# Optimization experiments

Hardware: AMD Instinct MI355X
Metric: run time of the kernel (lower is better)

Reference implementation:

```python
import jax, jax.numpy as jnp
import numpy as np

N_NODES = 100000
N_EDGES = 1600000
IN_DIM = 128
HEADS = 4
HEAD_DIM = 16  # hidden_dim 64 // 4 heads
HID = HEADS * HEAD_DIM
NEG_SLOPE = 0.2


def setup_inputs() -> dict:
    key = jax.random.key(0)
    ks = jax.random.split(key, 20)
    inp = {
        "x": jax.random.normal(ks[0], (N_NODES, IN_DIM), dtype=jnp.float32),
        "edge_index": jax.random.randint(ks[1], (2, N_EDGES), 0, N_NODES, dtype=jnp.int32),
    }
    dims = [IN_DIM, HID, HID]
    for l in range(3):
        d_in = dims[l]
        sc = 1.0 / np.sqrt(d_in)
        inp[f"w{l}"] = jax.random.normal(ks[2 + 4 * l], (d_in, HID), dtype=jnp.float32) * sc
        inp[f"asrc{l}"] = jax.random.normal(ks[3 + 4 * l], (HEADS, HEAD_DIM), dtype=jnp.float32) * 0.1
        inp[f"adst{l}"] = jax.random.normal(ks[4 + 4 * l], (HEADS, HEAD_DIM), dtype=jnp.float32) * 0.1
        inp[f"b{l}"] = jnp.zeros((HID,), dtype=jnp.float32)
    inp["out_w"] = jax.random.normal(ks[14], (HID, 1), dtype=jnp.float32) * (1.0 / np.sqrt(HID))
    inp["out_b"] = jnp.zeros((1,), dtype=jnp.float32)
    return inp


def _gat_layer(h, src, dst, W, a_src, a_dst, b):
    # h: [N, d_in]; src/dst: [E'] (self-loops already appended)
    n = h.shape[0]
    xh = (h @ W).reshape(n, HEADS, HEAD_DIM)              # [N,H,C]
    al_s = jnp.sum(xh * a_src, axis=-1)                   # [N,H]
    al_d = jnp.sum(xh * a_dst, axis=-1)                   # [N,H]
    e = jax.nn.leaky_relu(al_s[src] + al_d[dst], NEG_SLOPE)  # [E',H]
    # segment-softmax over incoming edges of each destination node
    m = jax.ops.segment_max(e, dst, num_segments=n)       # [N,H]
    p = jnp.exp(e - m[dst])
    z = jax.ops.segment_sum(p, dst, num_segments=n)       # [N,H]
    alpha = p / (z[dst] + 1e-16)                          # [E',H]
    msg = xh[src] * alpha[:, :, None]                     # [E',H,C]
    out = jax.ops.segment_sum(msg, dst, num_segments=n)   # [N,H,C]
    return out.reshape(n, HID) + b


def reference(x, edge_index, w0, asrc0, adst0, b0, w1, asrc1, adst1, b1,
              w2, asrc2, adst2, b2, out_w, out_b):
    n = x.shape[0]
    loops = jnp.arange(n, dtype=edge_index.dtype)
    src = jnp.concatenate([edge_index[0], loops])  # PyG GATConv adds self-loops
    dst = jnp.concatenate([edge_index[1], loops])
    h = x
    params = [(w0, asrc0, adst0, b0), (w1, asrc1, adst1, b1), (w2, asrc2, adst2, b2)]
    for W, a_s, a_d, b in params:
        h = _gat_layer(h, src, dst, W, a_s, a_d, b)
        h = jax.nn.relu(h)
    return (h @ out_w + out_b).squeeze(-1)  # [N]
```

## Files before the change

kernel.cpp:

```cpp
#include <hip/hip_runtime.h>


#define NBMAX 512
#define SCHUNK 4096
#define BCAP 8192

typedef __attribute__((ext_vector_type(8))) short bf16x8;
typedef __attribute__((ext_vector_type(4))) float f32x4;

__device__ inline unsigned short bf16_rtn(float x) {
    union { float f; unsigned u; } a; a.f = x;
    return (unsigned short)((a.u + 0x7FFFu + ((a.u >> 16) & 1u)) >> 16);
}
__device__ inline float bf16_to_f(unsigned short s) {
    union { unsigned u; float f; } b; b.u = ((unsigned)s) << 16;
    return b.f;
}

__global__ __launch_bounds__(256) void k_zero(int* p, int n) {
    int i = blockIdx.x * 256 + threadIdx.x;
    if (i < n) p[i] = 0;
}

__global__ __launch_bounds__(256) void k_bhist(const int* __restrict__ dst, int* __restrict__ bhist, int e) {
    __shared__ unsigned int h[NBMAX];
    int t = threadIdx.x;
    h[t] = 0;
    h[t + 256] = 0;
    __syncthreads();
    for (int i = blockIdx.x * 256 + t; i < e; i += gridDim.x * 256)
        atomicAdd(&h[dst[i] >> 8], 1u);
    __syncthreads();
    if (h[t]) atomicAdd(&bhist[t], (int)h[t]);
    if (h[t + 256]) atomicAdd(&bhist[t + 256], (int)h[t + 256]);
}

__global__ __launch_bounds__(512) void k_bscan(const int* __restrict__ bhist, int* __restrict__ boffs,
                                               int* __restrict__ bfill, int nb, int e) {
    __shared__ int s[NBMAX];
    int t = threadIdx.x;
    int v = (t < nb) ? bhist[t] : 0;
    s[t] = v;
    __syncthreads();
    for (int o = 1; o < 512; o <<= 1) {
        int add = (t >= o) ? s[t - o] : 0;
        __syncthreads();
        s[t] += add;
        __syncthreads();
    }
    boffs[t] = s[t] - v;
    if (t == 511) boffs[512] = s[511];
    bfill[t] = 0;
}

__global__ __launch_bounds__(512) void k_bscatter(const int* __restrict__ src, const int* __restrict__ dst,
                                                  const int* __restrict__ boffs, int* __restrict__ bfill,
                                                  unsigned int* __restrict__ edata, int e) {
    __shared__ unsigned int hist[NBMAX];
    __shared__ unsigned int loc[NBMAX];
    __shared__ int gbase[NBMAX];
    __shared__ unsigned int stmp[NBMAX];
    __shared__ unsigned int sortbuf[SCHUNK];
    __shared__ int posbuf[SCHUNK];
    int t = threadIdx.x;
    int i0 = blockIdx.x * SCHUNK;
    int cnt = min(SCHUNK, e - i0);
    hist[t] = 0;
    __syncthreads();
    for (int j = t; j < cnt; j += 512) atomicAdd(&hist[dst[i0 + j] >> 8], 1u);
    __syncthreads();
    unsigned int v = hist[t];
    stmp[t] = v;
    __syncthreads();
    for (int o = 1; o < 512; o <<= 1) {
        unsigned int add = (t >= o) ? stmp[t - o] : 0;
        __syncthreads();
        stmp[t] += add;
        __syncthreads();
    }
    loc[t] = stmp[t] - v;
    int gb = 0;
    if (v > 0) gb = atomicAdd(&bfill[t], (int)v);
    gbase[t] = boffs[t] + gb - (int)loc[t];
    hist[t] = loc[t];
    __syncthreads();
    for (int j = t; j < cnt; j += 512) {
        int d = dst[i0 + j];
        int s = src[i0 + j];
        int b = d >> 8;
        unsigned int p = atomicAdd(&hist[b], 1u);
        sortbuf[p] = (unsigned int)s | ((unsigned int)(d & 255) << 24);
        posbuf[p] = gbase[b] + (int)p;
    }
    __syncthreads();
    for (int j = t; j < cnt; j += 512) edata[posbuf[j]] = sortbuf[j];
}

__global__ __launch_bounds__(256) void k_bfinal(const unsigned int* __restrict__ edata,
                                                const int* __restrict__ boffs, int* __restrict__ offs,
                                                int* __restrict__ ssrc, int* __restrict__ sdst,
                                                int n, int nb) {
    __shared__ unsigned int hist[256];
    __shared__ unsigned int stmp[256];
    __shared__ unsigned int loc[256];
    __shared__ unsigned int srcbuf[BCAP];
    __shared__ unsigned char dstbuf[BCAP];
    int b = blockIdx.x;
    int t = threadIdx.x;
    int e0 = boffs[b], e1 = boffs[b + 1];
    int cnt = e1 - e0;
    hist[t] = 0;
    __syncthreads();
    for (int j = t; j < cnt; j += 256) atomicAdd(&hist[edata[e0 + j] >> 24], 1u);
    __syncthreads();
    unsigned int v = hist[t];
    stmp[t] = v;
    __syncthreads();
    for (int o = 1; o < 256; o <<= 1) {
        unsigned int add = (t >= o) ? stmp[t - o] : 0;
        __syncthreads();
        stmp[t] += add;
        __syncthreads();
    }
    loc[t] = stmp[t] - v;
    int node = b * 256 + t;
    if (node < n) offs[node] = e0 + (int)loc[t];
    if (b == nb - 1 && t == 0) offs[n] = e1;
    hist[t] = loc[t];
    __syncthreads();
    if (cnt <= BCAP) {
        for (int j = t; j < cnt; j += 256) {
            unsigned int p = edata[e0 + j];
            unsigned int pos = atomicAdd(&hist[p >> 24], 1u);
            srcbuf[pos] = p & 0xFFFFFFu;
            dstbuf[pos] = (unsigned char)(p >> 24);
        }
        __syncthreads();
        for (int j = t; j < cnt; j += 256) {
            ssrc[e0 + j] = (int)srcbuf[j];
            sdst[e0 + j] = b * 256 + (int)dstbuf[j];
        }
    } else {
        for (int j = t; j < cnt; j += 256) {
            unsigned int p = edata[e0 + j];
            unsigned int pos = atomicAdd(&hist[p >> 24], 1u);
            ssrc[e0 + (int)pos] = (int)(p & 0xFFFFFFu);
            sdst[e0 + (int)pos] = b * 256 + (int)(p >> 24);
        }
    }
}

__global__ __launch_bounds__(256) void k_wprep(const float* __restrict__ w0, const float* __restrict__ w1,
                                               const float* __restrict__ w2,
                                               unsigned short* __restrict__ p0h, unsigned short* __restrict__ p0l,
                                               unsigned short* __restrict__ p1h, unsigned short* __restrict__ p1l,
                                               unsigned short* __restrict__ p2h, unsigned short* __restrict__ p2l) {
    int g = blockIdx.x * 256 + threadIdx.x;
    const float* W;
    unsigned short *ph, *pl;
    int idx;
    if (g < 1024) { W = w0; ph = p0h; pl = p0l; idx = g; }
    else if (g < 1536) { W = w1; ph = p1h; pl = p1l; idx = g - 1024; }
    else if (g < 2048) { W = w2; ph = p2h; pl = p2l; idx = g - 1536; }
    else return;
    int ko = idx >> 6, nn = idx & 63;
#pragma unroll
    for (int j = 0; j < 8; ++j) {
        float w = W[(size_t)(ko * 8 + j) * 64 + nn];
        unsigned short hb = bf16_rtn(w);
        ph[(size_t)idx * 8 + j] = hb;
        pl[(size_t)idx * 8 + j] = bf16_rtn(w - bf16_to_f(hb));
    }
}

template <int D_IN>
__global__ __launch_bounds__(256) void k_mgemm(const float* __restrict__ h,
                                               const unsigned short* __restrict__ wph,
                                               const unsigned short* __restrict__ wpl,
                                               const float* __restrict__ asrc, const float* __restrict__ adst,
                                               float* __restrict__ xh, float* __restrict__ als,
                                               float* __restrict__ ald, int n) {
    int t = threadIdx.x;
    int wv = t >> 6, lane = t & 63;
    int quad = lane >> 4, l16 = lane & 15;
    int m0 = blockIdx.x * 64 + wv * 16;
    int node_a = m0 + l16;
    int mm = min(node_a, n - 1);
    const float* hrow = h + (size_t)mm * D_IN + quad * 8;

    f32x4 acc[4];
#pragma unroll
    for (int i = 0; i < 4; ++i) acc[i] = (f32x4){0.f, 0.f, 0.f, 0.f};

    constexpr int KSTEPS = D_IN / 32;
#pragma unroll
    for (int s = 0; s < KSTEPS; ++s) {
        float4 a0 = *(const float4*)(hrow + s * 32);
        float4 a1 = *(const float4*)(hrow + s * 32 + 4);
        float av[8] = {a0.x, a0.y, a0.z, a0.w, a1.x, a1.y, a1.z, a1.w};
        bf16x8 ahi, alo;
#pragma unroll
        for (int j = 0; j < 8; ++j) {
            unsigned short hb = bf16_rtn(av[j]);
            ahi[j] = (short)hb;
            alo[j] = (short)bf16_rtn(av[j] - bf16_to_f(hb));
        }
        const unsigned short* bbase = wph + ((size_t)((s * 4 + quad) * 64 + l16)) * 8;
        const unsigned short* bbasel = wpl + ((size_t)((s * 4 + quad) * 64 + l16)) * 8;
#pragma unroll
        for (int nt = 0; nt < 4; ++nt) {
            bf16x8 bhi = *(const bf16x8*)(bbase + (size_t)nt * 16 * 8);
            bf16x8 blo = *(const bf16x8*)(bbasel + (size_t)nt * 16 * 8);
            acc[nt] = __builtin_amdgcn_mfma_f32_16x16x32_bf16(ahi, bhi, acc[nt], 0, 0, 0);
            acc[nt] = __builtin_amdgcn_mfma_f32_16x16x32_bf16(ahi, blo, acc[nt], 0, 0, 0);
            acc[nt] = __builtin_amdgcn_mfma_f32_16x16x32_bf16(alo, bhi, acc[nt], 0, 0, 0);
        }
    }
#pragma unroll
    for (int nt = 0; nt < 4; ++nt) {
        float as_l = asrc[nt * 16 + l16];
        float ad_l = adst[nt * 16 + l16];
#pragma unroll
        for (int r = 0; r < 4; ++r) {
            int node = m0 + quad * 4 + r;
            float c = acc[nt][r];
            if (node < n) xh[(size_t)node * 64 + nt * 16 + l16] = c;
            float ps = c * as_l, pd = c * ad_l;
            ps += __shfl_xor(ps, 1, 64); pd += __shfl_xor(pd, 1, 64);
            ps += __shfl_xor(ps, 2, 64); pd += __shfl_xor(pd, 2, 64);
            ps += __shfl_xor(ps, 4, 64); pd += __shfl_xor(pd, 4, 64);
            ps += __shfl_xor(ps, 8, 64); pd += __shfl_xor(pd, 8, 64);
            if (l16 == 0 && node < n) {
                als[node * 4 + nt] = ps;
                ald[node * 4 + nt] = pd;
            }
        }
    }
}

__device__ inline float4 lrelu4(float4 v) {
    float4 r;
    r.x = v.x >= 0.f ? v.x : 0.2f * v.x;
    r.y = v.y >= 0.f ? v.y : 0.2f * v.y;
    r.z = v.z >= 0.f ? v.z : 0.2f * v.z;
    r.w = v.w >= 0.f ? v.w : 0.2f * v.w;
    return r;
}

__global__ __launch_bounds__(256) void k_edge(const int* __restrict__ ssrc, const int* __restrict__ sdst,
                                              const float* __restrict__ als, const float* __restrict__ ald,
                                              float* __restrict__ pei, int e) {
    int j = blockIdx.x * 256 + threadIdx.x;
    if (j >= e) return;
    int u = ssrc[j], d = sdst[j];
    float4 alu = *(const float4*)(als + 4 * (size_t)u);
    float4 asd = *(const float4*)(als + 4 * (size_t)d);
    float4 add4 = *(const float4*)(ald + 4 * (size_t)d);
    float4 m4 = lrelu4(make_float4(asd.x + add4.x, asd.y + add4.y, asd.z + add4.z, asd.w + add4.w));
    float4 e4 = lrelu4(make_float4(alu.x + add4.x, alu.y + add4.y, alu.z + add4.z, alu.w + add4.w));
    float4 pe;
    pe.x = __expf(e4.x - m4.x);
    pe.y = __expf(e4.y - m4.y);
    pe.z = __expf(e4.z - m4.z);
    pe.w = __expf(e4.w - m4.w);
    *(float4*)(pei + 4 * (size_t)j) = pe;
}

__global__ __launch_bounds__(256) void k_agg(const float* __restrict__ xh, const float* __restrict__ pei,
                                             const int* __restrict__ offs, const int* __restrict__ ssrc,
                                             const float* __restrict__ bias, float* __restrict__ hout,
                                             const float* __restrict__ outw, const float* __restrict__ outb,
                                             float* __restrict__ fout, int n) {
    __shared__ int s_u[4][64];
    __shared__ float s_pe[4][4][64];
    int wslot = threadIdx.x >> 6;
    int lane = threadIdx.x & 63;
    int v = (blockIdx.x * 256 + threadIdx.x) >> 6;
    if (v >= n) return;
    int head = lane >> 4;
    int* ub = s_u[wslot];
    float* per = s_pe[wslot][head];
    float* pew = &s_pe[wslot][0][lane];

    int start = offs[v], end = offs[v + 1];
    const char* xl = (const char*)(xh + lane);
    float acc = *(const float*)(xl + ((size_t)(unsigned)v << 8));
    float zsum = 0.f;

    for (int s0 = start; s0 < end; s0 += 64) {
        int cnt = min(64, end - s0);
        bool act = lane < cnt;
        int u = v;
        float4 pe = make_float4(0.f, 0.f, 0.f, 0.f);
        if (act) {
            u = ssrc[s0 + lane];
            pe = *(const float4*)(pei + 4 * (size_t)(s0 + lane));
        }
        ub[lane] = u << 8;
        pew[0] = pe.x;
        pew[64] = pe.y;
        pew[128] = pe.z;
        pew[192] = pe.w;
        int ng = (cnt + 3) >> 2;
        int g = 0;
        for (; g + 2 <= ng; g += 2) {
            int4 uu0 = *(const int4*)&ub[g * 4];
            int4 uu1 = *(const int4*)&ub[g * 4 + 4];
            float4 pp0 = *(const float4*)&per[g * 4];
            float4 pp1 = *(const float4*)&per[g * 4 + 4];
            float x0 = *(const float*)(xl + (size_t)(unsigned)uu0.x);
            float x1 = *(const float*)(xl + (size_t)(unsigned)uu0.y);
            float x2 = *(const float*)(xl + (size_t)(unsigned)uu0.z);
            float x3 = *(const float*)(xl + (size_t)(unsigned)uu0.w);
            float x4 = *(const float*)(xl + (size_t)(unsigned)uu1.x);
            float x5 = *(const float*)(xl + (size_t)(unsigned)uu1.y);
            float x6 = *(const float*)(xl + (size_t)(unsigned)uu1.z);
            float x7 = *(const float*)(xl + (size_t)(unsigned)uu1.w);
            zsum += pp0.x + pp0.y + pp0.z + pp0.w;
            zsum += pp1.x + pp1.y + pp1.z + pp1.w;
            acc += pp0.x * x0; acc += pp0.y * x1; acc += pp0.z * x2; acc += pp0.w * x3;
            acc += pp1.x * x4; acc += pp1.y * x5; acc += pp1.z * x6; acc += pp1.w * x7;
        }
        for (; g < ng; ++g) {
            int4 uu = *(const int4*)&ub[g * 4];
            float4 pp = *(const float4*)&per[g * 4];
            float x0 = *(const float*)(xl + (size_t)(unsigned)uu.x);
            float x1 = *(const float*)(xl + (size_t)(unsigned)uu.y);
            float x2 = *(const float*)(xl + (size_t)(unsigned)uu.z);
            float x3 = *(const float*)(xl + (size_t)(unsigned)uu.w);
            zsum += pp.x + pp.y + pp.z + pp.w;
            acc += pp.x * x0; acc += pp.y * x1; acc += pp.z * x2; acc += pp.w * x3;
        }
    }
    float z = 1.f + zsum;
    float o = acc / (z + 1e-16f) + bias[lane];
    o = fmaxf(o, 0.f);
    if (outw) {
        float tsum = o * outw[lane];
#pragma unroll
        for (int d = 32; d; d >>= 1) tsum += __shfl_down(tsum, d, 64);
        if (lane == 0) fout[v] = tsum + outb[0];
    } else {
        hout[((size_t)v << 6) + lane] = o;
    }
}

extern "C" void kernel_launch(void* const* d_in, const int* in_sizes, int n_in,
                              void* d_out, int out_size, void* d_ws, size_t ws_size,
                              hipStream_t stream) {
    const float* x = (const float*)d_in[0];
    const int* ei = (const int*)d_in[1];
    const float* w[3] = {(const float*)d_in[2], (const float*)d_in[6], (const float*)d_in[10]};
    const float* as[3] = {(const float*)d_in[3], (const float*)d_in[7], (const float*)d_in[11]};
    const float* ad[3] = {(const float*)d_in[4], (const float*)d_in[8], (const float*)d_in[12]};
    const float* b[3] = {(const float*)d_in[5], (const float*)d_in[9], (const float*)d_in[13]};
    const float* outw = (const float*)d_in[14];
    const float* outb = (const float*)d_in[15];

    const int N = in_sizes[0] / 128;
    const int E = in_sizes[1] / 2;
    const int* src = ei;
    const int* dst = ei + E;
    const int NB = (N + 255) / 256;

    char* ws = (char*)d_ws;
    auto alloc = [&](size_t bytes) -> void* {
        void* p = (void*)ws;
        ws += (bytes + 255) & ~(size_t)255;
        return p;
    };
    int* bhist = (int*)alloc(NBMAX * 4);
    int* boffs = (int*)alloc((NBMAX + 1) * 4);
    int* bfill = (int*)alloc(NBMAX * 4);
    int* offs = (int*)alloc((size_t)(N + 1) * 4);
    int* ssrc = (int*)alloc((size_t)E * 4);
    int* sdst = (int*)alloc((size_t)E * 4);
    float* pei = (float*)alloc((size_t)E * 4 * 4);
    float* xh = (float*)alloc((size_t)N * 64 * 4);
    float* hbuf = (float*)alloc((size_t)N * 64 * 4);
    float* als = (float*)alloc((size_t)N * 4 * 4);
    float* ald = (float*)alloc((size_t)N * 4 * 4);
    unsigned short* p0h = (unsigned short*)alloc(8192 * 2);
    unsigned short* p0l = (unsigned short*)alloc(8192 * 2);
    unsigned short* p1h = (unsigned short*)alloc(4096 * 2);
    unsigned short* p1l = (unsigned short*)alloc(4096 * 2);
    unsigned short* p2h = (unsigned short*)alloc(4096 * 2);
    unsigned short* p2l = (unsigned short*)alloc(4096 * 2);
    unsigned int* edata = (unsigned int*)xh;

    k_wprep<<<8, 256, 0, stream>>>(w[0], w[1], w[2], p0h, p0l, p1h, p1l, p2h, p2l);
    k_zero<<<(NBMAX + 255) / 256, 256, 0, stream>>>(bhist, NBMAX);
    k_bhist<<<256, 256, 0, stream>>>(dst, bhist, E);
    k_bscan<<<1, 512, 0, stream>>>(bhist, boffs, bfill, NB, E);
    k_bscatter<<<(E + SCHUNK - 1) / SCHUNK, 512, 0, stream>>>(src, dst, boffs, bfill, edata, E);
    k_bfinal<<<NB, 256, 0, stream>>>(edata, boffs, offs, ssrc, sdst, N, NB);

    const int gblocks = (N + 63) / 64;
    const int ablocks = (N + 3) / 4;
    const int eblocks = (E + 255) / 256;

    k_mgemm<128><<<gblocks, 256, 0, stream>>>(x, p0h, p0l, as[0], ad[0], xh, als, ald, N);
    k_edge<<<eblocks, 256, 0, stream>>>(ssrc, sdst, als, ald, pei, E);
    k_agg<<<ablocks, 256, 0, stream>>>(xh, pei, offs, ssrc, b[0], hbuf, nullptr, nullptr, nullptr, N);
    k_mgemm<64><<<gblocks, 256, 0, stream>>>(hbuf, p1h, p1l, as[1], ad[1], xh, als, ald, N);
    k_edge<<<eblocks, 256, 0, stream>>>(ssrc, sdst, als, ald, pei, E);
    k_agg<<<ablocks, 256, 0, stream>>>(xh, pei, offs, ssrc, b[1], hbuf, nullptr, nullptr, nullptr, N);
    k_mgemm<64><<<gblocks, 256, 0, stream>>>(hbuf, p2h, p2l, as[2], ad[2], xh, als, ald, N);
    k_edge<<<eblocks, 256, 0, stream>>>(ssrc, sdst, als, ald, pei, E);
    k_agg<<<ablocks, 256, 0, stream>>>(xh, pei, offs, ssrc, b[2], nullptr, outw, outb, (float*)d_out, N);
}
```

Measured before the change: 448.2 us.

## Fuse edge attention scoring into aggregation kernel and drop sdst/pei buffers

```diff
diff --git a/kernel.cpp b/kernel.cpp
--- a/kernel.cpp
+++ b/kernel.cpp
@@ -17,18 +17,38 @@
     return b.f;
 }
 
-__global__ __launch_bounds__(256) void k_zero(int* p, int n) {
-    int i = blockIdx.x * 256 + threadIdx.x;
-    if (i < n) p[i] = 0;
-}
-
-__global__ __launch_bounds__(256) void k_bhist(const int* __restrict__ dst, int* __restrict__ bhist, int e) {
+__global__ __launch_bounds__(256) void k_bhist_wprep(
+        const int* __restrict__ dst, int* __restrict__ bhist, int e,
+        const float* __restrict__ w0, const float* __restrict__ w1, const float* __restrict__ w2,
+        unsigned short* __restrict__ p0h, unsigned short* __restrict__ p0l,
+        unsigned short* __restrict__ p1h, unsigned short* __restrict__ p1l,
+        unsigned short* __restrict__ p2h, unsigned short* __restrict__ p2l) {
+    int t = threadIdx.x;
+    if (blockIdx.x < 8) {
+        int g = blockIdx.x * 256 + t;
+        const float* W;
+        unsigned short *ph, *pl;
+        int idx;
+        if (g < 1024) { W = w0; ph = p0h; pl = p0l; idx = g; }
+        else if (g < 1536) { W = w1; ph = p1h; pl = p1l; idx = g - 1024; }
+        else if (g < 2048) { W = w2; ph = p2h; pl = p2l; idx = g - 1536; }
+        else return;
+        int ko = idx >> 6, nn = idx & 63;
+#pragma unroll
+        for (int j = 0; j < 8; ++j) {
+            float w = W[(size_t)(ko * 8 + j) * 64 + nn];
+            unsigned short hb = bf16_rtn(w);
+            ph[(size_t)idx * 8 + j] = hb;
+            pl[(size_t)idx * 8 + j] = bf16_rtn(w - bf16_to_f(hb));
+        }
+        return;
+    }
     __shared__ unsigned int h[NBMAX];
-    int t = threadIdx.x;
     h[t] = 0;
     h[t + 256] = 0;
     __syncthreads();
-    for (int i = blockIdx.x * 256 + t; i < e; i += gridDim.x * 256)
+    int bid = blockIdx.x - 8;
+    for (int i = bid * 256 + t; i < e; i += 256 * 256)
         atomicAdd(&h[dst[i] >> 8], 1u);
     __syncthreads();
     if (h[t]) atomicAdd(&bhist[t], (int)h[t]);
@@ -98,13 +118,11 @@
 
 __global__ __launch_bounds__(256) void k_bfinal(const unsigned int* __restrict__ edata,
                                                 const int* __restrict__ boffs, int* __restrict__ offs,
-                                                int* __restrict__ ssrc, int* __restrict__ sdst,
-                                                int n, int nb) {
+                                                int* __restrict__ ssrc, int n, int nb) {
     __shared__ unsigned int hist[256];
     __shared__ unsigned int stmp[256];
     __shared__ unsigned int loc[256];
     __shared__ unsigned int srcbuf[BCAP];
-    __shared__ unsigned char dstbuf[BCAP];
     int b = blockIdx.x;
     int t = threadIdx.x;
     int e0 = boffs[b], e1 = boffs[b + 1];
@@ -133,43 +151,15 @@
             unsigned int p = edata[e0 + j];
             unsigned int pos = atomicAdd(&hist[p >> 24], 1u);
             srcbuf[pos] = p & 0xFFFFFFu;
-            dstbuf[pos] = (unsigned char)(p >> 24);
-        }
-        __syncthreads();
-        for (int j = t; j < cnt; j += 256) {
-            ssrc[e0 + j] = (int)srcbuf[j];
-            sdst[e0 + j] = b * 256 + (int)dstbuf[j];
-        }
+        }
+        __syncthreads();
+        for (int j = t; j < cnt; j += 256) ssrc[e0 + j] = (int)srcbuf[j];
     } else {
         for (int j = t; j < cnt; j += 256) {
             unsigned int p = edata[e0 + j];
             unsigned int pos = atomicAdd(&hist[p >> 24], 1u);
             ssrc[e0 + (int)pos] = (int)(p & 0xFFFFFFu);
-            sdst[e0 + (int)pos] = b * 256 + (int)(p >> 24);
-        }
-    }
-}
-
-__global__ __launch_bounds__(256) void k_wprep(const float* __restrict__ w0, const float* __restrict__ w1,
-                                               const float* __restrict__ w2,
-                                               unsigned short* __restrict__ p0h, unsigned short* __restrict__ p0l,
-                                               unsigned short* __restrict__ p1h, unsigned short* __restrict__ p1l,
-                                               unsigned short* __restrict__ p2h, unsigned short* __restrict__ p2l) {
-    int g = blockIdx.x * 256 + threadIdx.x;
-    const float* W;
-    unsigned short *ph, *pl;
-    int idx;
-    if (g < 1024) { W = w0; ph = p0h; pl = p0l; idx = g; }
-    else if (g < 1536) { W = w1; ph = p1h; pl = p1l; idx = g - 1024; }
-    else if (g < 2048) { W = w2; ph = p2h; pl = p2l; idx = g - 1536; }
-    else return;
-    int ko = idx >> 6, nn = idx & 63;
-#pragma unroll
-    for (int j = 0; j < 8; ++j) {
-        float w = W[(size_t)(ko * 8 + j) * 64 + nn];
-        unsigned short hb = bf16_rtn(w);
-        ph[(size_t)idx * 8 + j] = hb;
-        pl[(size_t)idx * 8 + j] = bf16_rtn(w - bf16_to_f(hb));
+        }
     }
 }
 
@@ -247,30 +237,11 @@
     return r;
 }
 
-__global__ __launch_bounds__(256) void k_edge(const int* __restrict__ ssrc, const int* __restrict__ sdst,
-                                              const float* __restrict__ als, const float* __restrict__ ald,
-                                              float* __restrict__ pei, int e) {
-    int j = blockIdx.x * 256 + threadIdx.x;
-    if (j >= e) return;
-    int u = ssrc[j], d = sdst[j];
-    float4 alu = *(const float4*)(als + 4 * (size_t)u);
-    float4 asd = *(const float4*)(als + 4 * (size_t)d);
-    float4 add4 = *(const float4*)(ald + 4 * (size_t)d);
-    float4 m4 = lrelu4(make_float4(asd.x + add4.x, asd.y + add4.y, asd.z + add4.z, asd.w + add4.w));
-    float4 e4 = lrelu4(make_float4(alu.x + add4.x, alu.y + add4.y, alu.z + add4.z, alu.w + add4.w));
-    float4 pe;
-    pe.x = __expf(e4.x - m4.x);
-    pe.y = __expf(e4.y - m4.y);
-    pe.z = __expf(e4.z - m4.z);
-    pe.w = __expf(e4.w - m4.w);
-    *(float4*)(pei + 4 * (size_t)j) = pe;
-}
-
-__global__ __launch_bounds__(256) void k_agg(const float* __restrict__ xh, const float* __restrict__ pei,
-                                             const int* __restrict__ offs, const int* __restrict__ ssrc,
-                                             const float* __restrict__ bias, float* __restrict__ hout,
-                                             const float* __restrict__ outw, const float* __restrict__ outb,
-                                             float* __restrict__ fout, int n) {
+__global__ __launch_bounds__(256) void k_agg(const float* __restrict__ xh, const float* __restrict__ als,
+                                             const float* __restrict__ ald, const int* __restrict__ offs,
+                                             const int* __restrict__ ssrc, const float* __restrict__ bias,
+                                             float* __restrict__ hout, const float* __restrict__ outw,
+                                             const float* __restrict__ outb, float* __restrict__ fout, int n) {
     __shared__ int s_u[4][64];
     __shared__ float s_pe[4][4][64];
     int wslot = threadIdx.x >> 6;
@@ -283,31 +254,46 @@
     float* pew = &s_pe[wslot][0][lane];
 
     int start = offs[v], end = offs[v + 1];
+    float4 ald4 = *(const float4*)(ald + 4 * (size_t)v);
+    float4 als4v = *(const float4*)(als + 4 * (size_t)v);
+    float4 m4 = lrelu4(make_float4(als4v.x + ald4.x, als4v.y + ald4.y, als4v.z + ald4.z, als4v.w + ald4.w));
+
     const char* xl = (const char*)(xh + lane);
-    float acc = *(const float*)(xl + ((size_t)(unsigned)v << 8));
-    float zsum = 0.f;
+    float acc0 = *(const float*)(xl + ((size_t)(unsigned)v << 8));
+    float acc1 = 0.f;
+    float zs0 = 0.f, zs1 = 0.f;
 
     for (int s0 = start; s0 < end; s0 += 64) {
         int cnt = min(64, end - s0);
         bool act = lane < cnt;
         int u = v;
-        float4 pe = make_float4(0.f, 0.f, 0.f, 0.f);
+        float4 alu = make_float4(-1e30f, -1e30f, -1e30f, -1e30f);
         if (act) {
             u = ssrc[s0 + lane];
-            pe = *(const float4*)(pei + 4 * (size_t)(s0 + lane));
-        }
+            alu = *(const float4*)(als + 4 * (size_t)u);
+        }
+        float4 e4 = lrelu4(make_float4(alu.x + ald4.x, alu.y + ald4.y, alu.z + ald4.z, alu.w + ald4.w));
+        float4 pe;
+        pe.x = __expf(e4.x - m4.x);
+        pe.y = __expf(e4.y - m4.y);
+        pe.z = __expf(e4.z - m4.z);
+        pe.w = __expf(e4.w - m4.w);
         ub[lane] = u << 8;
         pew[0] = pe.x;
         pew[64] = pe.y;
         pew[128] = pe.z;
         pew[192] = pe.w;
-        int ng = (cnt + 3) >> 2;
+        int ngp = (cnt + 3) >> 2;
         int g = 0;
-        for (; g + 2 <= ng; g += 2) {
+        for (; g + 4 <= ngp; g += 4) {
             int4 uu0 = *(const int4*)&ub[g * 4];
             int4 uu1 = *(const int4*)&ub[g * 4 + 4];
+            int4 uu2 = *(const int4*)&ub[g * 4 + 8];
+            int4 uu3 = *(const int4*)&ub[g * 4 + 12];
             float4 pp0 = *(const float4*)&per[g * 4];
             float4 pp1 = *(const float4*)&per[g * 4 + 4];
+            float4 pp2 = *(const float4*)&per[g * 4 + 8];
+            float4 pp3 = *(const float4*)&per[g * 4 + 12];
             float x0 = *(const float*)(xl + (size_t)(unsigned)uu0.x);
             float x1 = *(const float*)(xl + (size_t)(unsigned)uu0.y);
             float x2 = *(const float*)(xl + (size_t)(unsigned)uu0.z);
@@ -316,24 +302,34 @@
             float x5 = *(const float*)(xl + (size_t)(unsigned)uu1.y);
             float x6 = *(const float*)(xl + (size_t)(unsigned)uu1.z);
             float x7 = *(const float*)(xl + (size_t)(unsigned)uu1.w);
-            zsum += pp0.x + pp0.y + pp0.z + pp0.w;
-            zsum += pp1.x + pp1.y + pp1.z + pp1.w;
-            acc += pp0.x * x0; acc += pp0.y * x1; acc += pp0.z * x2; acc += pp0.w * x3;
-            acc += pp1.x * x4; acc += pp1.y * x5; acc += pp1.z * x6; acc += pp1.w * x7;
-        }
-        for (; g < ng; ++g) {
+            float x8 = *(const float*)(xl + (size_t)(unsigned)uu2.x);
+            float x9 = *(const float*)(xl + (size_t)(unsigned)uu2.y);
+            float xa = *(const float*)(xl + (size_t)(unsigned)uu2.z);
+            float xb = *(const float*)(xl + (size_t)(unsigned)uu2.w);
+            float xc = *(const float*)(xl + (size_t)(unsigned)uu3.x);
+            float xd = *(const float*)(xl + (size_t)(unsigned)uu3.y);
+            float xe = *(const float*)(xl + (size_t)(unsigned)uu3.z);
+            float xf = *(const float*)(xl + (size_t)(unsigned)uu3.w);
+            zs0 += (pp0.x + pp0.y) + (pp0.z + pp0.w) + (pp2.x + pp2.y) + (pp2.z + pp2.w);
+            zs1 += (pp1.x + pp1.y) + (pp1.z + pp1.w) + (pp3.x + pp3.y) + (pp3.z + pp3.w);
+            acc0 += pp0.x * x0; acc0 += pp0.y * x1; acc0 += pp0.z * x2; acc0 += pp0.w * x3;
+            acc1 += pp1.x * x4; acc1 += pp1.y * x5; acc1 += pp1.z * x6; acc1 += pp1.w * x7;
+            acc0 += pp2.x * x8; acc0 += pp2.y * x9; acc0 += pp2.z * xa; acc0 += pp2.w * xb;
+            acc1 += pp3.x * xc; acc1 += pp3.y * xd; acc1 += pp3.z * xe; acc1 += pp3.w * xf;
+        }
+        for (; g < ngp; ++g) {
             int4 uu = *(const int4*)&ub[g * 4];
             float4 pp = *(const float4*)&per[g * 4];
             float x0 = *(const float*)(xl + (size_t)(unsigned)uu.x);
             float x1 = *(const float*)(xl + (size_t)(unsigned)uu.y);
             float x2 = *(const float*)(xl + (size_t)(unsigned)uu.z);
             float x3 = *(const float*)(xl + (size_t)(unsigned)uu.w);
-            zsum += pp.x + pp.y + pp.z + pp.w;
-            acc += pp.x * x0; acc += pp.y * x1; acc += pp.z * x2; acc += pp.w * x3;
-        }
-    }
-    float z = 1.f + zsum;
-    float o = acc / (z + 1e-16f) + bias[lane];
+            zs0 += (pp.x + pp.y) + (pp.z + pp.w);
+            acc0 += pp.x * x0; acc0 += pp.y * x1; acc0 += pp.z * x2; acc0 += pp.w * x3;
+        }
+    }
+    float z = 1.f + zs0 + zs1;
+    float o = (acc0 + acc1) / (z + 1e-16f) + bias[lane];
     o = fmaxf(o, 0.f);
     if (outw) {
         float tsum = o * outw[lane];
@@ -374,8 +370,6 @@
     int* bfill = (int*)alloc(NBMAX * 4);
     int* offs = (int*)alloc((size_t)(N + 1) * 4);
     int* ssrc = (int*)alloc((size_t)E * 4);
-    int* sdst = (int*)alloc((size_t)E * 4);
-    float* pei = (float*)alloc((size_t)E * 4 * 4);
     float* xh = (float*)alloc((size_t)N * 64 * 4);
     float* hbuf = (float*)alloc((size_t)N * 64 * 4);
     float* als = (float*)alloc((size_t)N * 4 * 4);
@@ -388,24 +382,20 @@
     unsigned short* p2l = (unsigned short*)alloc(4096 * 2);
     unsigned int* edata = (unsigned int*)xh;
 
-    k_wprep<<<8, 256, 0, stream>>>(w[0], w[1], w[2], p0h, p0l, p1h, p1l, p2h, p2l);
-    k_zero<<<(NBMAX + 255) / 256, 256, 0, stream>>>(bhist, NBMAX);
-    k_bhist<<<256, 256, 0, stream>>>(dst, bhist, E);
+    hipMemsetAsync(bhist, 0, NBMAX * 4, stream);
+    k_bhist_wprep<<<264, 256, 0, stream>>>(dst, bhist, E, w[0], w[1], w[2],
+                                           p0h, p0l, p1h, p1l, p2h, p2l);
     k_bscan<<<1, 512, 0, stream>>>(bhist, boffs, bfill, NB, E);
     k_bscatter<<<(E + SCHUNK - 1) / SCHUNK, 512, 0, stream>>>(src, dst, boffs, bfill, edata, E);
-    k_bfinal<<<NB, 256, 0, stream>>>(edata, boffs, offs, ssrc, sdst, N, NB);
+    k_bfinal<<<NB, 256, 0, stream>>>(edata, boffs, offs, ssrc, N, NB);
 
     const int gblocks = (N + 63) / 64;
     const int ablocks = (N + 3) / 4;
-    const int eblocks = (E + 255) / 256;
 
     k_mgemm<128><<<gblocks, 256, 0, stream>>>(x, p0h, p0l, as[0], ad[0], xh, als, ald, N);
-    k_edge<<<eblocks, 256, 0, stream>>>(ssrc, sdst, als, ald, pei, E);
-    k_agg<<<ablocks, 256, 0, stream>>>(xh, pei, offs, ssrc, b[0], hbuf, nullptr, nullptr, nullptr, N);
+    k_agg<<<ablocks, 256, 0, stream>>>(xh, als, ald, offs, ssrc, b[0], hbuf, nullptr, nullptr, nullptr, N);
     k_mgemm<64><<<gblocks, 256, 0, stream>>>(hbuf, p1h, p1l, as[1], ad[1], xh, als, ald, N);
-    k_edge<<<eblocks, 256, 0, stream>>>(ssrc, sdst, als, ald, pei, E);
-    k_agg<<<ablocks, 256, 0, stream>>>(xh, pei, offs, ssrc, b[1], hbuf, nullptr, nullptr, nullptr, N);
+    k_agg<<<ablocks, 256, 0, stream>>>(xh, als, ald, offs, ssrc, b[1], hbuf, nullptr, nullptr, nullptr, N);
     k_mgemm<64><<<gblocks, 256, 0, stream>>>(hbuf, p2h, p2l, as[2], ad[2], xh, als, ald, N);
-    k_edge<<<eblocks, 256, 0, stream>>>(ssrc, sdst, als, ald, pei, E);
-    k_agg<<<ablocks, 256, 0, stream>>>(xh, pei, offs, ssrc, b[2], nullptr, outw, outb, (float*)d_out, N);
-}
+    k_agg<<<ablocks, 256, 0, stream>>>(xh, als, ald, offs, ssrc, b[2], nullptr, outw, outb, (float*)d_out, N);
+}
```

Result: slower. 465.6 us (+3.9%).
